# Optimization experiments

Measured on AMD Instinct MI355X. Metric: run time of the kernel, lower is better.

## Reference

```python
import jax, jax.numpy as jnp
import numpy as np

N_NODES = 50000
N_EDGES = 1600000
IN_C = 64
OUT_C = 64
N_CLASSES = 45


def setup_inputs() -> dict:
    key = jax.random.key(0)
    ks = jax.random.split(key, 12)

    def lin(k, i, o):
        return jax.random.normal(k, (i, o), jnp.float32) / np.float32(np.sqrt(i))

    return dict(
        x=jax.random.normal(ks[0], (N_NODES, IN_C), jnp.float32),
        edge_index=jax.random.randint(ks[1], (2, N_EDGES), 0, N_NODES, dtype=jnp.int32),
        W_z=lin(ks[2], IN_C, OUT_C), b_z=jnp.zeros((OUT_C,), jnp.float32),
        Wl_z=lin(ks[3], 2 * OUT_C, OUT_C), bl_z=jnp.zeros((OUT_C,), jnp.float32),
        W_r=lin(ks[4], IN_C, OUT_C), b_r=jnp.zeros((OUT_C,), jnp.float32),
        Wl_r=lin(ks[5], 2 * OUT_C, OUT_C), bl_r=jnp.zeros((OUT_C,), jnp.float32),
        W_h=lin(ks[6], IN_C, OUT_C), b_h=jnp.zeros((OUT_C,), jnp.float32),
        Wl_h=lin(ks[7], 2 * OUT_C, OUT_C), bl_h=jnp.zeros((OUT_C,), jnp.float32),
        W_out=lin(ks[8], OUT_C, N_CLASSES), b_out=jnp.zeros((N_CLASSES,), jnp.float32),
    )


def _gcn(x, W, b, src, dst, dinv):
    # GCNConv with improved self-loops (fill value 2.0):
    # out = D^{-1/2} (A + 2I) D^{-1/2} X W + b, with deg = in_degree + 2
    xw = x @ W                                   # [N, OUT_C]
    norm = dinv[src] * dinv[dst]                 # [E]
    agg = jax.ops.segment_sum(norm[:, None] * xw[src], dst, num_segments=N_NODES)
    agg = agg + (2.0 * dinv * dinv)[:, None] * xw  # self-loop contribution
    return agg + b


def reference(x, edge_index, W_z, b_z, Wl_z, bl_z, W_r, b_r, Wl_r, bl_r,
              W_h, b_h, Wl_h, bl_h, W_out, b_out):
    src, dst = edge_index[0], edge_index[1]
    deg = jax.ops.segment_sum(jnp.ones((N_EDGES,), jnp.float32), dst,
                              num_segments=N_NODES) + 2.0
    dinv = jax.lax.rsqrt(deg)

    # TGCN cell with H0 = 0 (no prior hidden state passed)
    H = jnp.zeros((N_NODES, OUT_C), x.dtype)
    Z = jax.nn.sigmoid(
        jnp.concatenate([_gcn(x, W_z, b_z, src, dst, dinv), H], axis=1) @ Wl_z + bl_z)
    R = jax.nn.sigmoid(
        jnp.concatenate([_gcn(x, W_r, b_r, src, dst, dinv), H], axis=1) @ Wl_r + bl_r)
    H_tilde = jnp.tanh(
        jnp.concatenate([_gcn(x, W_h, b_h, src, dst, dinv), H * R], axis=1) @ Wl_h + bl_h)
    H = Z * H + (1.0 - Z) * H_tilde

    # relu + linear readout to 45 classes
    return jax.nn.relu(H) @ W_out + b_out
```

## Files before the change

### kernel.cpp

```cpp
#include <hip/hip_runtime.h>

#define N_NODES 50000
#define N_EDGES 1600000
#define NB 782
#define NBB 256
#define CHUNK 6250
#define CAP 2560
#define SCAP 3072
#define ZROW 50000
#define NTILES 3125

typedef unsigned short ushort_t;
typedef _Float16 v8h __attribute__((ext_vector_type(8)));
typedef _Float16 v4h __attribute__((ext_vector_type(4)));
typedef _Float16 v2h __attribute__((ext_vector_type(2)));
typedef float f32x4_t __attribute__((ext_vector_type(4)));


__global__ __launch_bounds__(256) void k_binw(
    const int* __restrict__ ei, int* __restrict__ gcur, int* __restrict__ bins,
    const float* __restrict__ Wz, const float* __restrict__ bz,
    const float* __restrict__ Wlz, const float* __restrict__ blz,
    const float* __restrict__ Wh, const float* __restrict__ bh,
    const float* __restrict__ Wlh, const float* __restrict__ blh,
    const float* __restrict__ Wout, float* __restrict__ B2f,
    _Float16* __restrict__ Bzh, _Float16* __restrict__ Bwo) {
  __shared__ int arena[9120];
  int tid = threadIdx.x, blk = blockIdx.x;
  if (blk < NBB) {
    int* h      = arena;
    int* lo     = arena + NB;
    int* segb   = arena + 2 * NB;
    int* ssum   = arena + 3 * NB;
    int* sorted = arena + 3 * NB + 512;
    for (int i = tid; i < NB; i += 256) h[i] = 0;
    __syncthreads();
    const int2* s2 = (const int2*)(ei + blk * CHUNK);
    const int2* d2 = (const int2*)(ei + N_EDGES + blk * CHUNK);
    for (int i = tid; i < CHUNK / 2; i += 256) {
      int2 d = d2[i];
      atomicAdd(&h[d.x >> 6], 1);
      atomicAdd(&h[d.y >> 6], 1);
    }
    __syncthreads();
    for (int b = tid; b < NB; b += 256) {
      int c = h[b];
      segb[b] = c ? atomicAdd(&gcur[b], c) : 0;
    }
    int bi = tid * 4;
    int v0 = (bi < NB) ? h[bi] : 0;
    int v1 = (bi + 1 < NB) ? h[bi + 1] : 0;
    int v2 = (bi + 2 < NB) ? h[bi + 2] : 0;
    int v3 = (bi + 3 < NB) ? h[bi + 3] : 0;
    int ts = v0 + v1 + v2 + v3;
    ssum[tid] = ts;
    __syncthreads();
    for (int off = 1; off < 256; off <<= 1) {
      int u = (tid >= off) ? ssum[tid - off] : 0;
      __syncthreads();
      ssum[tid] += u;
      __syncthreads();
    }
    int ex = ssum[tid] - ts;
    if (bi < NB)     { lo[bi] = ex;     ex += v0; }
    if (bi + 1 < NB) { lo[bi + 1] = ex; ex += v1; }
    if (bi + 2 < NB) { lo[bi + 2] = ex; ex += v2; }
    if (bi + 3 < NB) { lo[bi + 3] = ex; }
    __syncthreads();
    for (int b = tid; b < NB; b += 256) h[b] = lo[b];
    __syncthreads();
    for (int i = tid; i < CHUNK / 2; i += 256) {
      int2 s = s2[i];
      int2 d = d2[i];
      int vx = s.x | ((d.x & 63) << 16) | ((d.x >> 6) << 22);
      int vy = s.y | ((d.y & 63) << 16) | ((d.y >> 6) << 22);
      int px = atomicAdd(&h[(unsigned)vx >> 22], 1);
      sorted[px] = vx;
      int py = atomicAdd(&h[(unsigned)vy >> 22], 1);
      sorted[py] = vy;
    }
    __syncthreads();
    for (int t = tid; t < CHUNK; t += 256) {
      int v = sorted[t];
      int b = (unsigned)v >> 22;
      bins[b * CAP + segb[b] + (t - lo[b])] = v & 0x3FFFFF;
    }
  } else {
    int wblk = blk - NBB;
    float* A  = (float*)arena;
    float* Bm = (float*)(arena + 4160);
    bool zpath = wblk < 4;
    const float* Wsrc = zpath ? Wz : Wh;
    const float* Lsrc = zpath ? Wlz : Wlh;
    for (int idx = tid; idx < 4096; idx += 256) {
      A[(idx >> 6) * 65 + (idx & 63)] = Wsrc[idx];
      Bm[(idx >> 6) * 65 + (idx & 63)] = Lsrc[idx];
    }
    __syncthreads();
    int lane = (tid >> 1) & 63;
    int j0 = (tid & 1) * 4;
    int ks = (tid >> 7) & 1;
    int k0 = ks * 32 + ((lane >> 4) << 3) + j0;
    int col = (wblk & 3) * 16 + (lane & 15);
    float a0 = 0.f, a1 = 0.f, a2 = 0.f, a3 = 0.f;
    for (int q = 0; q < 64; ++q) {
      float bv = Bm[q * 65 + col];
      a0 = fmaf(A[k0 * 65 + q], bv, a0);
      a1 = fmaf(A[(k0 + 1) * 65 + q], bv, a1);
      a2 = fmaf(A[(k0 + 2) * 65 + q], bv, a2);
      a3 = fmaf(A[(k0 + 3) * 65 + q], bv, a3);
    }
    int tb = wblk * 1024 + tid * 4;
    v4h o; o[0] = (_Float16)a0; o[1] = (_Float16)a1;
    o[2] = (_Float16)a2; o[3] = (_Float16)a3;
    *(v4h*)(Bzh + tb) = o;
    if ((wblk == 0 || wblk == 4) && tid < 64) {
      float v = zpath ? blz[tid] : blh[tid];
      const float* bb = zpath ? bz : bh;
      for (int q = 0; q < 64; ++q) v = fmaf(bb[q], Bm[q * 65 + tid], v);
      B2f[tid * 2 + (zpath ? 0 : 1)] = v;
    }
    if (wblk == 1) {
      for (int e2 = 0; e2 < 12; ++e2) {
        int t2 = tid * 12 + e2;
        int ln = (t2 >> 3) & 63, j = t2 & 7;
        int ntile = t2 >> 10, ks2 = (t2 >> 9) & 1;
        int n = ntile * 16 + (ln & 15);
        int k = ks2 * 32 + ((ln >> 4) << 3) + j;
        Bwo[t2] = (_Float16)((n < 45) ? Wout[k * 45 + n] : 0.f);
      }
    }
  }
}

__global__ __launch_bounds__(256, 4) void k_sort(
    const int* __restrict__ bins, const int* __restrict__ gcur,
    const float* __restrict__ x,
    ushort_t* __restrict__ srcp, int2* __restrict__ rowiv,
    float* __restrict__ dinv, _Float16* __restrict__ xp) {
  __shared__ int dg[64], lo[64], cur[64];
  __shared__ float sdin[64];
  __shared__ int Tsh;
  __shared__ ushort_t buf[8192];
  int tid = threadIdx.x, b = blockIdx.x;
  int start = b * CAP, end = start + gcur[b];
  if (tid < 64) dg[tid] = 0;
  __syncthreads();
  for (int i = start + tid; i < end; i += 256)
    atomicAdd(&dg[bins[i] >> 16], 1);
  __syncthreads();
  int pdv = 0;
  if (tid < 64) { pdv = (dg[tid] + 7) & ~7; lo[tid] = pdv; }
  __syncthreads();
  for (int off = 1; off < 64; off <<= 1) {
    int u = 0;
    if (tid < 64 && tid >= off) u = lo[tid - off];
    __syncthreads();
    if (tid < 64) lo[tid] += u;
    __syncthreads();
  }
  int ex = 0;
  if (tid < 64) {
    ex = lo[tid] - pdv;
    cur[tid] = ex;
    if (tid == 63) Tsh = lo[63];
  }
  __syncthreads();
  int T = Tsh;
  int base = b * SCAP;
  for (int i = tid; i < T; i += 256) buf[i] = (ushort_t)ZROW;
  __syncthreads();
  for (int i = start + tid; i < end; i += 256) {
    int v = bins[i];
    int dl = v >> 16;
    int p = atomicAdd(&cur[dl], 1);
    buf[p] = (ushort_t)(v & 0xFFFF);
  }
  __syncthreads();
  for (int i = tid; i < T; i += 256) srcp[base + i] = buf[i];
  if (tid < 64) {
    int v = b * 64 + tid;
    if (v < N_NODES) {
      rowiv[v] = make_int2(base + ex, pdv);
      float dv = rsqrtf((float)dg[tid] + 2.0f);
      dinv[v] = dv;
      sdin[tid] = dv;
    } else {
      sdin[tid] = 0.f;
    }
  }
  __syncthreads();
  const float4* x4 = (const float4*)x;
  int base4 = b * 1024;
  int nb64 = b * 4096;
  for (int idx = tid; idx < 1024; idx += 256) {
    int row = idx >> 4;
    int v = b * 64 + row;
    if (v < N_NODES) {
      float4 xv = x4[base4 + idx];
      float s = sdin[row];
      v4h o;
      o[0] = (_Float16)(s * xv.x); o[1] = (_Float16)(s * xv.y);
      o[2] = (_Float16)(s * xv.z); o[3] = (_Float16)(s * xv.w);
      *(v4h*)(xp + nb64 + idx * 4) = o;
    }
  }
  if (b == 0 && tid < 64) xp[ZROW * 64 + tid] = (_Float16)0.f;
}

__global__ __launch_bounds__(256, 8) void k_agg(
    const ushort_t* __restrict__ srcp, const int2* __restrict__ rowiv,
    const float* __restrict__ dinv, const _Float16* __restrict__ xp,
    _Float16* __restrict__ sxg) {
  int tid = threadIdx.x;
  int lane = tid & 63;
  int grp = lane >> 3;
  int chOff = (lane & 7) << 3;
  const v2h onE = {(_Float16)1.0f, (_Float16)0.0f};
  const v2h onO = {(_Float16)0.0f, (_Float16)1.0f};
  int w = blockIdx.x * 4 + (tid >> 6);
  int nw = gridDim.x * 4;
  for (int v = w; v < N_NODES; v += nw) {
    int vu = __builtin_amdgcn_readfirstlane(v);
    int2 ri = rowiv[vu];
    int beg = ri.x, pd = ri.y;
    float aE[2][4], aO[2][4];
    #pragma unroll
    for (int j = 0; j < 4; ++j) {
      aE[0][j] = 0.f; aE[1][j] = 0.f; aO[0][j] = 0.f; aO[1][j] = 0.f;
    }
    int e = beg, eend = beg + pd;
    for (; e + 32 <= eend; e += 32) {
      int s0 = (int)srcp[e + grp];
      int s1 = (int)srcp[e + 8 + grp];
      int s2 = (int)srcp[e + 16 + grp];
      int s3 = (int)srcp[e + 24 + grp];
      v8h r0 = *(const v8h*)(xp + (s0 << 6) + chOff);
      v8h r1 = *(const v8h*)(xp + (s1 << 6) + chOff);
      v8h r2 = *(const v8h*)(xp + (s2 << 6) + chOff);
      v8h r3 = *(const v8h*)(xp + (s3 << 6) + chOff);
      const v2h* p0 = (const v2h*)&r0;
      const v2h* p1 = (const v2h*)&r1;
      const v2h* p2 = (const v2h*)&r2;
      const v2h* p3 = (const v2h*)&r3;
      #pragma unroll
      for (int j = 0; j < 4; ++j) {
        aE[0][j] = __builtin_amdgcn_fdot2(p0[j], onE, aE[0][j], false);
        aO[0][j] = __builtin_amdgcn_fdot2(p0[j], onO, aO[0][j], false);
        aE[1][j] = __builtin_amdgcn_fdot2(p1[j], onE, aE[1][j], false);
        aO[1][j] = __builtin_amdgcn_fdot2(p1[j], onO, aO[1][j], false);
        aE[0][j] = __builtin_amdgcn_fdot2(p2[j], onE, aE[0][j], false);
        aO[0][j] = __builtin_amdgcn_fdot2(p2[j], onO, aO[0][j], false);
        aE[1][j] = __builtin_amdgcn_fdot2(p3[j], onE, aE[1][j], false);
        aO[1][j] = __builtin_amdgcn_fdot2(p3[j], onO, aO[1][j], false);
      }
    }
    for (; e < eend; e += 8) {
      int s0 = (int)srcp[e + grp];
      v8h r0 = *(const v8h*)(xp + (s0 << 6) + chOff);
      const v2h* p0 = (const v2h*)&r0;
      #pragma unroll
      for (int j = 0; j < 4; ++j) {
        aE[0][j] = __builtin_amdgcn_fdot2(p0[j], onE, aE[0][j], false);
        aO[0][j] = __builtin_amdgcn_fdot2(p0[j], onO, aO[0][j], false);
      }
    }
    float a[8];
    #pragma unroll
    for (int j = 0; j < 4; ++j) {
      a[2 * j]     = aE[0][j] + aE[1][j];
      a[2 * j + 1] = aO[0][j] + aO[1][j];
    }
    #pragma unroll
    for (int j = 0; j < 8; ++j) {
      a[j] += __shfl_xor(a[j], 8);
      a[j] += __shfl_xor(a[j], 16);
      a[j] += __shfl_xor(a[j], 32);
    }
    if (lane < 8) {
      float dv = dinv[vu];
      v8h self = *(const v8h*)(xp + (vu << 6) + chOff);
      v8h o;
      #pragma unroll
      for (int j = 0; j < 8; ++j)
        o[j] = (_Float16)(dv * a[j] + 2.f * dv * (float)self[j]);
      *(v8h*)(sxg + (vu << 6) + chOff) = o;
    }
  }
}

__global__ __launch_bounds__(256) void k_cell(
    const _Float16* __restrict__ sxg, const _Float16* __restrict__ Bzh,
    const _Float16* __restrict__ Bwo, const float2* __restrict__ B2,
    const float* __restrict__ bout, float* __restrict__ out) {
  __shared__ __align__(16) _Float16 tbuf[4][16][72];
  int tid = threadIdx.x;
  int lane = tid & 63, wv = tid >> 6;
  int l15 = lane & 15, quad = lane >> 4;
  int tile = blockIdx.x * 4 + wv;
  if (tile >= NTILES) return;

  v8h bzf[8][2], bwf[3][2];
  #pragma unroll
  for (int t = 0; t < 8; ++t)
    #pragma unroll
    for (int ks = 0; ks < 2; ++ks)
      bzf[t][ks] = *(const v8h*)(Bzh + (((t * 2 + ks) * 64 + lane) << 3));
  #pragma unroll
  for (int t = 0; t < 3; ++t)
    #pragma unroll
    for (int ks = 0; ks < 2; ++ks)
      bwf[t][ks] = *(const v8h*)(Bwo + (((t * 2 + ks) * 64 + lane) << 3));
  float zb[4], hb[4], ob[3];
  #pragma unroll
  for (int t = 0; t < 4; ++t) {
    float2 bb = B2[t * 16 + l15];
    zb[t] = bb.x; hb[t] = bb.y;
  }
  #pragma unroll
  for (int t = 0; t < 3; ++t) {
    int c = t * 16 + l15;
    ob[t] = (c < 45) ? bout[c] : 0.f;
  }

  const _Float16* ar = sxg + (tile * 16 + l15) * 64 + quad * 8;
  v8h a0 = *(const v8h*)ar;
  v8h a1 = *(const v8h*)(ar + 32);

  f32x4_t accz[8];
  #pragma unroll
  for (int t = 0; t < 8; ++t) {
    f32x4_t c4 = {0.f, 0.f, 0.f, 0.f};
    c4 = __builtin_amdgcn_mfma_f32_16x16x32_f16(a0, bzf[t][0], c4, 0, 0, 0);
    c4 = __builtin_amdgcn_mfma_f32_16x16x32_f16(a1, bzf[t][1], c4, 0, 0, 0);
    accz[t] = c4;
  }

  #pragma unroll
  for (int t = 0; t < 4; ++t) {
    #pragma unroll
    for (int r = 0; r < 4; ++r) {
      float zv = accz[t][r] + zb[t];
      float hv = accz[t + 4][r] + hb[t];
      float Z = 1.f / (1.f + __expf(-zv));
      float tt = fminf(15.f, fmaxf(-15.f, hv));
      float e2 = __expf(-2.f * tt);
      float Th = (1.f - e2) / (1.f + e2);
      tbuf[wv][quad * 4 + r][t * 16 + l15] = (_Float16)fmaxf((1.f - Z) * Th, 0.f);
    }
  }
  __asm__ volatile("s_waitcnt lgkmcnt(0)" ::: "memory");

  v8h p0 = *(const v8h*)&tbuf[wv][l15][quad * 8];
  v8h p1 = *(const v8h*)&tbuf[wv][l15][32 + quad * 8];

  #pragma unroll
  for (int t = 0; t < 3; ++t) {
    f32x4_t o4 = {0.f, 0.f, 0.f, 0.f};
    o4 = __builtin_amdgcn_mfma_f32_16x16x32_f16(p0, bwf[t][0], o4, 0, 0, 0);
    o4 = __builtin_amdgcn_mfma_f32_16x16x32_f16(p1, bwf[t][1], o4, 0, 0, 0);
    int c = t * 16 + l15;
    if (c < 45) {
      #pragma unroll
      for (int r = 0; r < 4; ++r)
        out[(tile * 16 + quad * 4 + r) * 45 + c] = o4[r] + ob[t];
    }
  }
}

extern "C" void kernel_launch(void* const* d_in, const int* in_sizes, int n_in,
                              void* d_out, int out_size, void* d_ws, size_t ws_size,
                              hipStream_t stream) {
  const float* x    = (const float*)d_in[0];
  const int*   ei   = (const int*)d_in[1];
  const float* Wz   = (const float*)d_in[2];
  const float* bz   = (const float*)d_in[3];
  const float* Wlz  = (const float*)d_in[4];
  const float* blz  = (const float*)d_in[5];
  const float* Wh   = (const float*)d_in[10];
  const float* bh   = (const float*)d_in[11];
  const float* Wlh  = (const float*)d_in[12];
  const float* blh  = (const float*)d_in[13];
  const float* Wout = (const float*)d_in[14];
  const float* bout = (const float*)d_in[15];
  float* out = (float*)d_out;

  char* w = (char*)d_ws;
  int*      bins  = (int*)(w + 0);
  _Float16* sxg   = (_Float16*)(w + 0);
  int*      gcur  = (int*)(w + 8007680);
  ushort_t* srcp  = (ushort_t*)(w + 8010816);
  int2*     rowiv = (int2*)(w + 12815424);
  float*    dinv  = (float*)(w + 13215424);
  float2*   B2    = (float2*)(w + 13415424);
  _Float16* Bzh   = (_Float16*)(w + 13415936);
  _Float16* Bwo   = (_Float16*)(w + 13432320);
  _Float16* xp    = (_Float16*)(w + 13438464);

  hipMemsetAsync(gcur, 0, NB * sizeof(int), stream);
  k_binw <<<NBB + 8, 256, 0, stream>>>(ei, gcur, bins, Wz, bz, Wlz, blz,
                                       Wh, bh, Wlh, blh, Wout,
                                       (float*)B2, Bzh, Bwo);
  k_sort <<<NB, 256, 0, stream>>>(bins, gcur, x, srcp, rowiv, dinv, xp);
  k_agg  <<<2048, 256, 0, stream>>>(srcp, rowiv, dinv, xp, sxg);
  k_cell <<<NB, 256, 0, stream>>>(sxg, Bzh, Bwo, B2, bout, out);
}
```

Measured before the change: 156.9 us.

## Replace global atomic bin cursors with fixed per-block bin slots and counts

```diff
diff --git a/kernel.cpp b/kernel.cpp
--- a/kernel.cpp
+++ b/kernel.cpp
@@ -5,7 +5,7 @@
 #define NB 782
 #define NBB 256
 #define CHUNK 6250
-#define CAP 2560
+#define CAPB 32
 #define SCAP 3072
 #define ZROW 50000
 #define NTILES 3125
@@ -18,21 +18,20 @@
 
 
 __global__ __launch_bounds__(256) void k_binw(
-    const int* __restrict__ ei, int* __restrict__ gcur, int* __restrict__ bins,
+    const int* __restrict__ ei, int* __restrict__ bins, int* __restrict__ cnt,
     const float* __restrict__ Wz, const float* __restrict__ bz,
     const float* __restrict__ Wlz, const float* __restrict__ blz,
     const float* __restrict__ Wh, const float* __restrict__ bh,
     const float* __restrict__ Wlh, const float* __restrict__ blh,
     const float* __restrict__ Wout, float* __restrict__ B2f,
     _Float16* __restrict__ Bzh, _Float16* __restrict__ Bwo) {
-  __shared__ int arena[9120];
+  __shared__ int arena[8320];
   int tid = threadIdx.x, blk = blockIdx.x;
   if (blk < NBB) {
     int* h      = arena;
     int* lo     = arena + NB;
-    int* segb   = arena + 2 * NB;
-    int* ssum   = arena + 3 * NB;
-    int* sorted = arena + 3 * NB + 512;
+    int* ssum   = arena + 1564;
+    int* sorted = arena + 2048;
     for (int i = tid; i < NB; i += 256) h[i] = 0;
     __syncthreads();
     const int2* s2 = (const int2*)(ei + blk * CHUNK);
@@ -43,10 +42,6 @@
       atomicAdd(&h[d.y >> 6], 1);
     }
     __syncthreads();
-    for (int b = tid; b < NB; b += 256) {
-      int c = h[b];
-      segb[b] = c ? atomicAdd(&gcur[b], c) : 0;
-    }
     int bi = tid * 4;
     int v0 = (bi < NB) ? h[bi] : 0;
     int v1 = (bi + 1 < NB) ? h[bi + 1] : 0;
@@ -83,8 +78,9 @@
     for (int t = tid; t < CHUNK; t += 256) {
       int v = sorted[t];
       int b = (unsigned)v >> 22;
-      bins[b * CAP + segb[b] + (t - lo[b])] = v & 0x3FFFFF;
-    }
+      bins[(b << 13) + (blk << 5) + (t - lo[b])] = v & 0x3FFFFF;
+    }
+    for (int b = tid; b < NB; b += 256) cnt[(b << 8) + blk] = h[b] - lo[b];
   } else {
     int wblk = blk - NBB;
     float* A  = (float*)arena;
@@ -134,20 +130,22 @@
 }
 
 __global__ __launch_bounds__(256, 4) void k_sort(
-    const int* __restrict__ bins, const int* __restrict__ gcur,
+    const int* __restrict__ bins, const int* __restrict__ cnt,
     const float* __restrict__ x,
     ushort_t* __restrict__ srcp, int2* __restrict__ rowiv,
     float* __restrict__ dinv, _Float16* __restrict__ xp) {
   __shared__ int dg[64], lo[64], cur[64];
   __shared__ float sdin[64];
   __shared__ int Tsh;
+  __shared__ int scnt[256];
   __shared__ ushort_t buf[8192];
   int tid = threadIdx.x, b = blockIdx.x;
-  int start = b * CAP, end = start + gcur[b];
+  scnt[tid] = cnt[(b << 8) + tid];
   if (tid < 64) dg[tid] = 0;
   __syncthreads();
-  for (int i = start + tid; i < end; i += 256)
-    atomicAdd(&dg[bins[i] >> 16], 1);
+  int bb = b << 13;
+  for (int i = tid; i < NBB * CAPB; i += 256)
+    if ((i & 31) < scnt[i >> 5]) atomicAdd(&dg[bins[bb + i] >> 16], 1);
   __syncthreads();
   int pdv = 0;
   if (tid < 64) { pdv = (dg[tid] + 7) & ~7; lo[tid] = pdv; }
@@ -170,11 +168,12 @@
   int base = b * SCAP;
   for (int i = tid; i < T; i += 256) buf[i] = (ushort_t)ZROW;
   __syncthreads();
-  for (int i = start + tid; i < end; i += 256) {
-    int v = bins[i];
-    int dl = v >> 16;
-    int p = atomicAdd(&cur[dl], 1);
-    buf[p] = (ushort_t)(v & 0xFFFF);
+  for (int i = tid; i < NBB * CAPB; i += 256) {
+    if ((i & 31) < scnt[i >> 5]) {
+      int v = bins[bb + i];
+      int p = atomicAdd(&cur[v >> 16], 1);
+      buf[p] = (ushort_t)(v & 0xFFFF);
+    }
   }
   __syncthreads();
   for (int i = tid; i < T; i += 256) srcp[base + i] = buf[i];
@@ -388,20 +387,19 @@
   char* w = (char*)d_ws;
   int*      bins  = (int*)(w + 0);
   _Float16* sxg   = (_Float16*)(w + 0);
-  int*      gcur  = (int*)(w + 8007680);
-  ushort_t* srcp  = (ushort_t*)(w + 8010816);
-  int2*     rowiv = (int2*)(w + 12815424);
-  float*    dinv  = (float*)(w + 13215424);
-  float2*   B2    = (float2*)(w + 13415424);
-  _Float16* Bzh   = (_Float16*)(w + 13415936);
-  _Float16* Bwo   = (_Float16*)(w + 13432320);
-  _Float16* xp    = (_Float16*)(w + 13438464);
-
-  hipMemsetAsync(gcur, 0, NB * sizeof(int), stream);
-  k_binw <<<NBB + 8, 256, 0, stream>>>(ei, gcur, bins, Wz, bz, Wlz, blz,
+  int*      cnt   = (int*)(w + 25624576);
+  ushort_t* srcp  = (ushort_t*)(w + 26425344);
+  int2*     rowiv = (int2*)(w + 31229952);
+  float*    dinv  = (float*)(w + 31629952);
+  float2*   B2    = (float2*)(w + 31829952);
+  _Float16* Bzh   = (_Float16*)(w + 31830464);
+  _Float16* Bwo   = (_Float16*)(w + 31846848);
+  _Float16* xp    = (_Float16*)(w + 31852992);
+
+  k_binw <<<NBB + 8, 256, 0, stream>>>(ei, bins, cnt, Wz, bz, Wlz, blz,
                                        Wh, bh, Wlh, blh, Wout,
                                        (float*)B2, Bzh, Bwo);
-  k_sort <<<NB, 256, 0, stream>>>(bins, gcur, x, srcp, rowiv, dinv, xp);
+  k_sort <<<NB, 256, 0, stream>>>(bins, cnt, x, srcp, rowiv, dinv, xp);
   k_agg  <<<2048, 256, 0, stream>>>(srcp, rowiv, dinv, xp, sxg);
   k_cell <<<NB, 256, 0, stream>>>(sxg, Bzh, Bwo, B2, bout, out);
 }
```

New measurement: 170.6 us. 8.7% more time.
